# Kernel tuning notes

Measured on AMD Instinct MI355X. Metric: run time of the kernel, lower is better.

Reference implementation:

```python
import jax, jax.numpy as jnp
import numpy as np

E, H2, V = 128, 512, 50000  # embedding_size, hidden_size*2, output_size
H4 = 2 * H2


def _gru_cell(x, h, W_ih, W_hh, b_ih, b_hh):
    # PyTorch GRU cell: gates ordered (r, z, n)
    gi = x @ W_ih.T + b_ih
    gh = h @ W_hh.T + b_hh
    i_r, i_z, i_n = jnp.split(gi, 3, axis=-1)
    h_r, h_z, h_n = jnp.split(gh, 3, axis=-1)
    r = jax.nn.sigmoid(i_r + h_r)
    z = jax.nn.sigmoid(i_z + h_z)
    n = jnp.tanh(i_n + r * h_n)
    return (1.0 - z) * n + z * h


def setup_inputs() -> dict:
    key = jax.random.key(0)
    ks = jax.random.split(key, 24)
    B, T = 64, 400
    s = 0.02
    inp = {
        "input_ids": jax.random.randint(ks[0], (B, 1), 0, V),
        "pre_hidden": jax.random.normal(ks[1], (2, B, H2), jnp.float32),
        "encoder_outputs": jax.random.normal(ks[2], (B, T, H2), jnp.float32),
        "source_input": jax.random.randint(ks[3], (B, T), 0, V),
        "coverage_vector": jax.random.uniform(ks[4], (B, 1, T), jnp.float32),
        "emb_table": jax.random.normal(ks[5], (V, E), jnp.float32) * s,
        "W_ih0": jax.random.normal(ks[6], (3 * H2, E), jnp.float32) * s,
        "W_hh0": jax.random.normal(ks[7], (3 * H2, H2), jnp.float32) * s,
        "b_ih0": jnp.zeros((3 * H2,), jnp.float32),
        "b_hh0": jnp.zeros((3 * H2,), jnp.float32),
        "W_ih1": jax.random.normal(ks[8], (3 * H2, H2), jnp.float32) * s,
        "W_hh1": jax.random.normal(ks[9], (3 * H2, H2), jnp.float32) * s,
        "b_ih1": jnp.zeros((3 * H2,), jnp.float32),
        "b_hh1": jnp.zeros((3 * H2,), jnp.float32),
        "align_W": jax.random.normal(ks[10], (1, 3 * H2), jnp.float32) * s,
        "align_b": jnp.zeros((1,), jnp.float32),
        "cov_W": jax.random.normal(ks[11], (H2, 1), jnp.float32) * s,
        "cov_b": jnp.zeros((H2,), jnp.float32),
        "fc1_W": jax.random.normal(ks[12], (H4, H4), jnp.float32) * s,
        "fc1_b": jnp.zeros((H4,), jnp.float32),
        "fc2_W": jax.random.normal(ks[13], (V, H4), jnp.float32) * s,
        "fc2_b": jnp.zeros((V,), jnp.float32),
        "gen_W": jax.random.normal(ks[14], (1, H4 + E), jnp.float32) * s,
        "gen_b": jnp.zeros((1,), jnp.float32),
    }
    return inp


def reference(input_ids, pre_hidden, encoder_outputs, source_input, coverage_vector,
              emb_table, W_ih0, W_hh0, b_ih0, b_hh0, W_ih1, W_hh1, b_ih1, b_hh1,
              align_W, align_b, cov_W, cov_b, fc1_W, fc1_b, fc2_W, fc2_b, gen_W, gen_b):
    B, T = source_input.shape
    # embedding lookup (dropout omitted / eval mode)
    emb = emb_table[input_ids[:, 0]]                          # [B,E]
    # 2-layer GRU, single decode step
    h0 = _gru_cell(emb, pre_hidden[0], W_ih0, W_hh0, b_ih0, b_hh0)
    h1 = _gru_cell(h0, pre_hidden[1], W_ih1, W_hh1, b_ih1, b_hh1)
    current_hidden = jnp.stack([h0, h1], axis=0)              # [2,B,H2]
    s = h1                                                    # [B,H2]
    cov = coverage_vector[:, 0, :]                            # [B,T]
    # coverage projection: Linear(1 -> H2)
    cov_feat = cov[:, :, None] * cov_W[:, 0][None, None, :] + cov_b  # [B,T,H2]
    s_rep = jnp.broadcast_to(s[:, None, :], (B, T, s.shape[-1]))
    combine = jnp.concatenate([encoder_outputs, s_rep, cov_feat], axis=-1)  # [B,T,3*H2]
    scores = jnp.einsum('bti,i->bt', combine, align_W[0]) + align_b[0]
    attn = jax.nn.softmax(jnp.tanh(scores), axis=1)           # [B,T]
    # coverage loss: sum of elementwise min(attn, coverage)
    coverage_loss = jnp.sum(jnp.minimum(attn, cov))
    new_coverage = coverage_vector + attn[:, None, :]         # [B,1,T]
    context = jnp.einsum('bt,bth->bh', attn, encoder_outputs) # [B,H2]
    ni = jnp.tanh(jnp.concatenate([s, context], axis=-1) @ fc1_W.T + fc1_b)
    logits = ni @ fc2_W.T + fc2_b                             # [B,V]
    Pvocab = jax.nn.softmax(logits, axis=1)
    # vectorized copy distribution: scatter-add attention mass onto source token ids
    batch_idx = jnp.arange(B)[:, None]
    copy_prob = jnp.zeros((B, logits.shape[1]), logits.dtype).at[batch_idx, source_input].add(attn)
    gen_in = jnp.concatenate([context, s, emb], axis=-1)      # [B,H4+E]
    p_gen = jax.nn.sigmoid(gen_in @ gen_W.T + gen_b)          # [B,1]
    out = Pvocab * p_gen + copy_prob * (1.0 - p_gen)
    return (out, current_hidden, attn[:, None, :], copy_prob, new_coverage, coverage_loss)
```

## Files before the change

### kernel.cpp

```cpp
#include <hip/hip_runtime.h>
#include <hip/hip_bf16.h>
#include <cstddef>

#define BB 64
#define TT 400
#define EE 128
#define HH 512
#define H4 1024
#define VV 50000
#define NCH 8
#define LSTR 136

#define OFF_OUT     0
#define OFF_CURHID  (BB*VV)
#define OFF_ATTN    (OFF_CURHID + 2*BB*HH)
#define OFF_COPY    (OFF_ATTN + BB*TT)
#define OFF_NEWCOV  (OFF_COPY + BB*VV)
#define OFF_LOSS    (OFF_NEWCOV + BB*TT)

#define WS_S      0
#define WS_TS     (WS_S + BB*HH)
#define WS_ATTN   (WS_TS + BB*TT)
#define WS_NIB    (WS_ATTN + BB*TT)
#define WS_A1     (WS_NIB + BB*H4/2)
#define WS_AX0    (WS_A1 + BB*H4/2)
#define WS_AH0    (WS_AX0 + BB*EE/2)
#define WS_AH1    (WS_AH0 + BB*HH/2)
#define WS_AX1    (WS_AH1 + BB*HH/2)
#define WS_PGEN   (WS_AX1 + BB*HH/2)
#define WS_RM     (WS_PGEN + 64)
#define WS_RS     (WS_RM + 64)
#define WS_CTXP   (WS_RS + 64)
#define WS_LOGITS (WS_CTXP + BB*NCH*HH)

typedef __attribute__((ext_vector_type(8))) short short8v;
typedef __attribute__((ext_vector_type(4))) short short4v;
typedef __attribute__((ext_vector_type(4))) float f32x4;

__device__ __forceinline__ float wredsum(float v) {
#pragma unroll
  for (int o = 32; o > 0; o >>= 1) v += __shfl_down(v, o, 64);
  return v;
}
__device__ __forceinline__ float wredmax(float v) {
#pragma unroll
  for (int o = 32; o > 0; o >>= 1) v = fmaxf(v, __shfl_down(v, o, 64));
  return v;
}
__device__ __forceinline__ float dot4(float4 a, float4 b) {
  return a.x*b.x + a.y*b.y + a.z*b.z + a.w*b.w;
}
__device__ __forceinline__ float sigmoidf(float x) { return 1.f / (1.f + expf(-x)); }
__device__ __forceinline__ short bfh(float f) {
  union { __hip_bfloat16 h; short s; } u; u.h = __float2bfloat16(f); return u.s;
}
__device__ __forceinline__ float bf2f(short s) {
  union { unsigned int u; float f; } v; v.u = ((unsigned int)(unsigned short)s) << 16; return v.f;
}

__global__ void zero_prep_kernel(float* __restrict__ p, float* __restrict__ loss,
                                 float* __restrict__ rs,
                                 const float* __restrict__ embt, const int* __restrict__ ids,
                                 const float* __restrict__ preh,
                                 short* __restrict__ ax0, short* __restrict__ ah0,
                                 short* __restrict__ ah1) {
  int i = blockIdx.x * 256 + threadIdx.x;
  ((float4*)p)[i] = make_float4(0.f, 0.f, 0.f, 0.f);
  if (i == 0) loss[0] = 0.f;
  if (i < 64) rs[i] = 0.f;
  if (i < BB * EE) {
    int b = i >> 7, k = i & 127;
    ax0[i] = bfh(embt[(size_t)ids[b] * EE + k]);
  } else if (i < BB * EE + 2 * BB * HH) {
    int j = i - BB * EE;
    if (j < BB * HH) ah0[j] = bfh(preh[j]);
    else ah1[j - BB * HH] = bfh(preh[j]);
  }
}

template<int KX>
__global__ __launch_bounds__(768) void gru_mfma_kernel(
    const short* __restrict__ Ax, const short* __restrict__ Ah,
    const float* __restrict__ W_ih, const float* __restrict__ W_hh,
    const float* __restrict__ b_ih, const float* __restrict__ b_hh,
    const float* __restrict__ hprev,
    float* __restrict__ hout_f, float* __restrict__ hout_o,
    short* __restrict__ hout_b, int bstride) {
  __shared__ float Pf[12 * 256];
  const int w = threadIdx.x >> 6;
  const int lane = threadIdx.x & 63;
  const int r16 = lane & 15, kg = lane >> 4;
  const int j0 = (blockIdx.x & 31) * 16;
  const int bg = blockIdx.x >> 5;
  const int half = (w >= 6) ? 1 : 0;
  const int wv = w - half * 6;
  const int part = (wv >= 3) ? 1 : 0;
  const int g = wv - part * 3;
  const int K = part ? HH : KX;
  const int Kh = K >> 1;
  const float* Wm = part ? W_hh : W_ih;
  const short* Am = part ? Ah : Ax;

  f32x4 acc = {0.f, 0.f, 0.f, 0.f};
  const float* wp = Wm + (size_t)(g * HH + j0 + r16) * K + half * Kh + kg * 8;
  const short* ap = Am + (size_t)(bg * 16 + r16) * K + half * Kh + kg * 8;
#pragma unroll 4
  for (int k0 = 0; k0 < Kh; k0 += 32) {
    float4 w0 = *(const float4*)(wp + k0);
    float4 w1 = *(const float4*)(wp + k0 + 4);
    short8v a = *(const short8v*)(ap + k0);
    short8v bf;
    bf[0] = bfh(w0.x); bf[1] = bfh(w0.y); bf[2] = bfh(w0.z); bf[3] = bfh(w0.w);
    bf[4] = bfh(w1.x); bf[5] = bfh(w1.y); bf[6] = bfh(w1.z); bf[7] = bfh(w1.w);
    acc = __builtin_amdgcn_mfma_f32_16x16x32_bf16(a, bf, acc, 0, 0, 0);
  }
  float* pw = Pf + (half * 6 + part * 3 + g) * 256;
#pragma unroll
  for (int r = 0; r < 4; r++) pw[(kg * 4 + r) * 16 + r16] = acc[r];
  __syncthreads();
  if (w == 0) {
    int col = j0 + r16;
    float bir = b_ih[col] + b_hh[col];
    float biz = b_ih[HH + col] + b_hh[HH + col];
    float bin = b_ih[2 * HH + col], bhn = b_hh[2 * HH + col];
#pragma unroll
    for (int r = 0; r < 4; r++) {
      int m = kg * 4 + r;
      int row = bg * 16 + m;
      int o = m * 16 + r16;
      float ih_r = Pf[0 * 256 + o] + Pf[6 * 256 + o];
      float ih_z = Pf[1 * 256 + o] + Pf[7 * 256 + o];
      float ih_n = Pf[2 * 256 + o] + Pf[8 * 256 + o];
      float hh_r = Pf[3 * 256 + o] + Pf[9 * 256 + o];
      float hh_z = Pf[4 * 256 + o] + Pf[10 * 256 + o];
      float hh_n = Pf[5 * 256 + o] + Pf[11 * 256 + o];
      float rv = sigmoidf(ih_r + hh_r + bir);
      float zv = sigmoidf(ih_z + hh_z + biz);
      float nv = tanhf(ih_n + bin + rv * (hh_n + bhn));
      float h = (1.f - zv) * nv + zv * hprev[(size_t)row * HH + col];
      hout_f[(size_t)row * HH + col] = h;
      hout_o[(size_t)row * HH + col] = h;
      hout_b[(size_t)row * bstride + col] = bfh(h);
    }
  }
}

__global__ void scores_kernel(const float* __restrict__ enc, const float* __restrict__ cov,
                              const float* __restrict__ aW, const float* __restrict__ ab,
                              const float* __restrict__ covW, const float* __restrict__ covb,
                              const float* __restrict__ s, float* __restrict__ ts) {
  int b = blockIdx.y;
  int wid = threadIdx.x >> 6, lane = threadIdx.x & 63;
  int t = blockIdx.x * 4 + wid;
  int i8 = lane * 8;
  const float* e = enc + ((size_t)b * TT + t) * HH + i8;
  float4 a0 = *(const float4*)&aW[i8],        a1 = *(const float4*)&aW[i8 + 4];
  float4 b0 = *(const float4*)&aW[HH + i8],   b1 = *(const float4*)&aW[HH + i8 + 4];
  float4 c0 = *(const float4*)&aW[2*HH + i8], c1 = *(const float4*)&aW[2*HH + i8 + 4];
  float4 s0 = *(const float4*)&s[(size_t)b * HH + i8], s1 = *(const float4*)&s[(size_t)b * HH + i8 + 4];
  float4 w0 = *(const float4*)&covW[i8],      w1 = *(const float4*)&covW[i8 + 4];
  float4 v0 = *(const float4*)&covb[i8],      v1 = *(const float4*)&covb[i8 + 4];
  float covbt = cov[b * TT + t];
  float p1 = dot4(*(const float4*)&e[0], a0) + dot4(*(const float4*)&e[4], a1)
           + dot4(s0, b0) + dot4(s1, b1)
           + dot4(v0, c0) + dot4(v1, c1);
  float p2 = dot4(w0, c0) + dot4(w1, c1);
  float d = wredsum(p1 + covbt * p2);
  if (lane == 0) ts[b * TT + t] = tanhf(d + ab[0]);
}

__global__ void attn_kernel(const float* __restrict__ ts, const float* __restrict__ cov,
                            const int* __restrict__ src,
                            float* __restrict__ wattn, float* __restrict__ dout,
                            float* __restrict__ outc) {
  int b = blockIdx.x, tid = threadIdx.x;
  int lane = tid & 63, wid = tid >> 6;
  __shared__ float sred[8];
  __shared__ float bval[2];
  float v = (tid < TT) ? ts[b * TT + tid] : -1e30f;
  float wm = wredmax(v);
  if (lane == 0) sred[wid] = wm;
  __syncthreads();
  if (wid == 0) {
    float r = (lane < 8) ? sred[lane] : -1e30f;
    r = wredmax(r);
    if (lane == 0) bval[0] = r;
  }
  __syncthreads();
  float m = bval[0];
  float e = (tid < TT) ? expf(v - m) : 0.f;
  float wsm = wredsum(e);
  __syncthreads();
  if (lane == 0) sred[wid] = wsm;
  __syncthreads();
  if (wid == 0) {
    float r = (lane < 8) ? sred[lane] : 0.f;
    r = wredsum(r);
    if (lane == 0) bval[1] = r;
  }
  __syncthreads();
  float denom = bval[1];
  float a = e / denom;
  float lp = 0.f;
  if (tid < TT) {
    wattn[b * TT + tid] = a;
    dout[OFF_ATTN + b * TT + tid] = a;
    float c = cov[b * TT + tid];
    dout[OFF_NEWCOV + b * TT + tid] = c + a;
    lp = fminf(a, c);
    atomicAdd(&outc[(size_t)b * VV + src[b * TT + tid]], a);
  }
  float wl = wredsum(lp);
  __syncthreads();
  if (lane == 0) sred[wid] = wl;
  __syncthreads();
  if (wid == 0) {
    float r = (lane < 8) ? sred[lane] : 0.f;
    r = wredsum(r);
    if (lane == 0) atomicAdd(&dout[OFF_LOSS], r);
  }
}

__global__ void ctx_part_kernel(const float* __restrict__ enc, const float* __restrict__ attn,
                                float* __restrict__ ctxp) {
  int b = blockIdx.x, c = blockIdx.y;
  int h = threadIdx.x;
  __shared__ float as[TT / NCH];
  if (h < TT / NCH) as[h] = attn[b * TT + c * (TT / NCH) + h];
  __syncthreads();
  const float* e = enc + ((size_t)b * TT + c * (TT / NCH)) * HH + h;
  float acc = 0.f;
#pragma unroll 10
  for (int t = 0; t < TT / NCH; t++) acc += as[t] * e[(size_t)t * HH];
  ctxp[((size_t)b * NCH + c) * HH + h] = acc;
}

__global__ void ctxred_pgen_kernel(const float* __restrict__ ctxp, const float* __restrict__ s,
                                   const float* __restrict__ embt, const int* __restrict__ ids,
                                   const float* __restrict__ gW, const float* __restrict__ gb,
                                   short* __restrict__ a1, float* __restrict__ pgen) {
  int b = blockIdx.x, tid = threadIdx.x;
  int lane = tid & 63, wid = tid >> 6;
  __shared__ float sred[8];
  float acc = 0.f;
#pragma unroll
  for (int c = 0; c < NCH; c++) acc += ctxp[((size_t)b * NCH + c) * HH + tid];
  a1[(size_t)b * H4 + HH + tid] = bfh(acc);
  float part = acc * gW[tid] + s[b * HH + tid] * gW[HH + tid];
  if (tid < EE) part += embt[(size_t)ids[b] * EE + tid] * gW[2 * HH + tid];
  float w = wredsum(part);
  if (lane == 0) sred[wid] = w;
  __syncthreads();
  if (wid == 0) {
    float r = (lane < 8) ? sred[lane] : 0.f;
    r = wredsum(r);
    if (lane == 0) pgen[b] = sigmoidf(r + gb[0]);
  }
}

__global__ __launch_bounds__(256) void fc1_kernel(const short* __restrict__ a1,
                                                  const float* __restrict__ W,
                                                  const float* __restrict__ bias,
                                                  short* __restrict__ nib) {
  __shared__ float part[4096];
  const int w = threadIdx.x >> 6;
  const int lane = threadIdx.x & 63;
  const int r16 = lane & 15, kg = lane >> 4;
  const int v0 = blockIdx.x * 16;
  const int kb = w * 256;

  f32x4 acc0 = {0.f,0.f,0.f,0.f}, acc1 = {0.f,0.f,0.f,0.f};
  f32x4 acc2 = {0.f,0.f,0.f,0.f}, acc3 = {0.f,0.f,0.f,0.f};
  const float* wp = W + (size_t)(v0 + r16) * H4 + kb + kg * 8;
  const short* ap = a1 + (size_t)r16 * H4 + kb + kg * 8;
#pragma unroll 4
  for (int k0 = 0; k0 < 256; k0 += 32) {
    float4 w0 = *(const float4*)(wp + k0);
    float4 w1 = *(const float4*)(wp + k0 + 4);
    short8v a0 = *(const short8v*)(ap + k0);
    short8v a1v = *(const short8v*)(ap + 16 * H4 + k0);
    short8v a2 = *(const short8v*)(ap + 32 * H4 + k0);
    short8v a3 = *(const short8v*)(ap + 48 * H4 + k0);
    short8v bf;
    bf[0] = bfh(w0.x); bf[1] = bfh(w0.y); bf[2] = bfh(w0.z); bf[3] = bfh(w0.w);
    bf[4] = bfh(w1.x); bf[5] = bfh(w1.y); bf[6] = bfh(w1.z); bf[7] = bfh(w1.w);
    acc0 = __builtin_amdgcn_mfma_f32_16x16x32_bf16(a0, bf, acc0, 0, 0, 0);
    acc1 = __builtin_amdgcn_mfma_f32_16x16x32_bf16(a1v, bf, acc1, 0, 0, 0);
    acc2 = __builtin_amdgcn_mfma_f32_16x16x32_bf16(a2, bf, acc2, 0, 0, 0);
    acc3 = __builtin_amdgcn_mfma_f32_16x16x32_bf16(a3, bf, acc3, 0, 0, 0);
  }
  float* pb = part + w * 1024;
#pragma unroll
  for (int r = 0; r < 4; r++) {
    pb[(kg * 4 + r) * 16 + r16]      = acc0[r];
    pb[(16 + kg * 4 + r) * 16 + r16] = acc1[r];
    pb[(32 + kg * 4 + r) * 16 + r16] = acc2[r];
    pb[(48 + kg * 4 + r) * 16 + r16] = acc3[r];
  }
  __syncthreads();
  int idx = threadIdx.x * 4;
  int m = idx >> 4, c0 = idx & 15;
  f32x4 s0 = *(const f32x4*)(part + idx);
  f32x4 s1 = *(const f32x4*)(part + 1024 + idx);
  f32x4 s2 = *(const f32x4*)(part + 2048 + idx);
  f32x4 s3 = *(const f32x4*)(part + 3072 + idx);
  f32x4 bv = *(const f32x4*)(bias + v0 + c0);
  f32x4 o = s0 + s1 + s2 + s3 + bv;
#pragma unroll
  for (int j = 0; j < 4; j++)
    nib[(size_t)m * H4 + v0 + c0 + j] = bfh(tanhf(o[j]));
}

__global__ __launch_bounds__(256) void fc2_kernel(const short* __restrict__ nib,
                                                  const float* __restrict__ W,
                                                  const float* __restrict__ bias,
                                                  short* __restrict__ logits_bf,
                                                  float* __restrict__ rs) {
  __shared__ short Wl[64 * LSTR];
  __shared__ short Al[64 * LSTR];
  const int tid = threadIdx.x;
  const int w = tid >> 6, lane = tid & 63;
  const int r16 = lane & 15, kg = lane >> 4;
  const int v0 = blockIdx.x * 64;
  const int srow = tid >> 2, quad = tid & 3;
  const int vr = min(v0 + srow, VV - 1);

  f32x4 acc[4];
#pragma unroll
  for (int i = 0; i < 4; i++) acc[i] = (f32x4){0.f, 0.f, 0.f, 0.f};

  const float* wsrc = W + (size_t)vr * H4 + quad * 4;
  const short* asrc = nib + (size_t)srow * H4 + quad * 8;

  float4 wreg[8];
  short8v areg[4];
#pragma unroll
  for (int j = 0; j < 8; j++) wreg[j] = *(const float4*)(wsrc + j * 16);
#pragma unroll
  for (int j = 0; j < 4; j++) areg[j] = *(const short8v*)(asrc + j * 32);

  for (int ks = 0; ks < 8; ks++) {
    {
      char* dst = (char*)Wl + srow * (LSTR * 2) + quad * 8;
#pragma unroll
      for (int j = 0; j < 8; j++) {
        float4 f = wreg[j];
        short4v h; h[0] = bfh(f.x); h[1] = bfh(f.y); h[2] = bfh(f.z); h[3] = bfh(f.w);
        *(short4v*)(dst + j * 32) = h;
      }
      char* adst = (char*)Al + srow * (LSTR * 2) + quad * 16;
#pragma unroll
      for (int j = 0; j < 4; j++)
        *(short8v*)(adst + j * 64) = areg[j];
    }
    __syncthreads();
    if (ks < 7) {
      const float* ws2 = wsrc + (ks + 1) * 128;
      const short* as2 = asrc + (ks + 1) * 128;
#pragma unroll
      for (int j = 0; j < 8; j++) wreg[j] = *(const float4*)(ws2 + j * 16);
#pragma unroll
      for (int j = 0; j < 4; j++) areg[j] = *(const short8v*)(as2 + j * 32);
    }
#pragma unroll
    for (int s = 0; s < 4; s++) {
      short8v wf = *(const short8v*)((char*)Wl + (w * 16 + r16) * (LSTR * 2) + s * 64 + kg * 16);
#pragma unroll
      for (int i = 0; i < 4; i++) {
        short8v af = *(const short8v*)((char*)Al + (i * 16 + r16) * (LSTR * 2) + s * 64 + kg * 16);
        acc[i] = __builtin_amdgcn_mfma_f32_16x16x32_bf16(af, wf, acc[i], 0, 0, 0);
      }
    }
    __syncthreads();
  }

  float* sc = (float*)Wl;
#pragma unroll
  for (int i = 0; i < 4; i++)
#pragma unroll
    for (int r = 0; r < 4; r++)
      sc[(i * 16 + kg * 4 + r) * 64 + w * 16 + r16] = acc[i][r];
  __syncthreads();
  int m = tid >> 2, q = tid & 3;
  int colbase = v0 + q * 16;
  float esum = 0.f;
  if (colbase < VV) {
    const float* scp = sc + m * 64 + q * 16;
    short8v lo, hi;
#pragma unroll
    for (int j = 0; j < 8; j++) {
      short lb = bfh(scp[j] + bias[colbase + j]);
      lo[j] = lb;
      esum += expf(bf2f(lb));
    }
#pragma unroll
    for (int j = 0; j < 8; j++) {
      short lb = bfh(scp[8 + j] + bias[colbase + 8 + j]);
      hi[j] = lb;
      esum += expf(bf2f(lb));
    }
    *(short8v*)(logits_bf + (size_t)m * VV + colbase)     = lo;
    *(short8v*)(logits_bf + (size_t)m * VV + colbase + 8) = hi;
  }
  esum += __shfl_down(esum, 2, 4);
  esum += __shfl_down(esum, 1, 4);
  if (q == 0) atomicAdd(&rs[m], esum);
}

__global__ void final_kernel(const short* __restrict__ logits_bf, const float* __restrict__ rs,
                             const float* __restrict__ pgen,
                             const float* __restrict__ copy, float* __restrict__ out) {
  int i = blockIdx.x * 256 + threadIdx.x;
  int b = (i * 4) / VV;
  float p = pgen[b], s = rs[b];
  short4v l = ((const short4v*)logits_bf)[i];
  float4 c = ((const float4*)copy)[i];
  float q = 1.f - p;
  float ps = p / s;
  float4 o;
  o.x = expf(bf2f(l[0])) * ps + c.x * q;
  o.y = expf(bf2f(l[1])) * ps + c.y * q;
  o.z = expf(bf2f(l[2])) * ps + c.z * q;
  o.w = expf(bf2f(l[3])) * ps + c.w * q;
  ((float4*)out)[i] = o;
}

extern "C" void kernel_launch(void* const* d_in, const int* in_sizes, int n_in,
                              void* d_out, int out_size, void* d_ws, size_t ws_size,
                              hipStream_t stream) {
  const int*   ids  = (const int*)d_in[0];
  const float* preh = (const float*)d_in[1];
  const float* enc  = (const float*)d_in[2];
  const int*   src  = (const int*)d_in[3];
  const float* cov  = (const float*)d_in[4];
  const float* embt = (const float*)d_in[5];
  const float* Wih0 = (const float*)d_in[6];
  const float* Whh0 = (const float*)d_in[7];
  const float* bih0 = (const float*)d_in[8];
  const float* bhh0 = (const float*)d_in[9];
  const float* Wih1 = (const float*)d_in[10];
  const float* Whh1 = (const float*)d_in[11];
  const float* bih1 = (const float*)d_in[12];
  const float* bhh1 = (const float*)d_in[13];
  const float* aW   = (const float*)d_in[14];
  const float* ab   = (const float*)d_in[15];
  const float* covW = (const float*)d_in[16];
  const float* covb = (const float*)d_in[17];
  const float* f1W  = (const float*)d_in[18];
  const float* f1b  = (const float*)d_in[19];
  const float* f2W  = (const float*)d_in[20];
  const float* f2b  = (const float*)d_in[21];
  const float* gW   = (const float*)d_in[22];
  const float* gb   = (const float*)d_in[23];
  float* out = (float*)d_out;
  float* ws  = (float*)d_ws;

  zero_prep_kernel<<<3125, 256, 0, stream>>>(out + OFF_COPY, out + OFF_LOSS, ws + WS_RS,
                                             embt, ids, preh,
                                             (short*)(ws + WS_AX0), (short*)(ws + WS_AH0),
                                             (short*)(ws + WS_AH1));
  gru_mfma_kernel<EE><<<128, 768, 0, stream>>>(
      (const short*)(ws + WS_AX0), (const short*)(ws + WS_AH0),
      Wih0, Whh0, bih0, bhh0, preh,
      out + OFF_CURHID, out + OFF_CURHID, (short*)(ws + WS_AX1), HH);
  gru_mfma_kernel<HH><<<128, 768, 0, stream>>>(
      (const short*)(ws + WS_AX1), (const short*)(ws + WS_AH1),
      Wih1, Whh1, bih1, bhh1, preh + BB * HH,
      ws + WS_S, out + OFF_CURHID + BB * HH, (short*)(ws + WS_A1), H4);
  scores_kernel<<<dim3(100, 64), 256, 0, stream>>>(enc, cov, aW, ab, covW, covb,
                                                   ws + WS_S, ws + WS_TS);
  attn_kernel<<<64, 512, 0, stream>>>(ws + WS_TS, cov, src, ws + WS_ATTN, out,
                                      out + OFF_COPY);
  ctx_part_kernel<<<dim3(64, NCH), 512, 0, stream>>>(enc, ws + WS_ATTN, ws + WS_CTXP);
  ctxred_pgen_kernel<<<64, 512, 0, stream>>>(ws + WS_CTXP, ws + WS_S, embt, ids, gW, gb,
                                             (short*)(ws + WS_A1), ws + WS_PGEN);
  fc1_kernel<<<64, 256, 0, stream>>>((const short*)(ws + WS_A1), f1W, f1b,
                                     (short*)(ws + WS_NIB));
  fc2_kernel<<<782, 256, 0, stream>>>((const short*)(ws + WS_NIB), f2W, f2b,
                                      (short*)(ws + WS_LOGITS), ws + WS_RS);
  final_kernel<<<3125, 256, 0, stream>>>((const short*)(ws + WS_LOGITS), ws + WS_RS,
                                         ws + WS_PGEN, out + OFF_COPY, out);
}
```

Before: 127.8 us.

## Split attention score, hoist encoder dot into prep kernel, double-buffer fc2 weights

The attention score is split algebraically: the encoder·align_W part only depends on inputs, so it is computed early in the zero/prep kernel. The hidden-state and coverage terms reduce to per-batch scalars computed inside attn_kernel, which removes the separate scores_kernel launch and takes it off the GRU-dependent critical path. Separately, fc2 now keeps two register buffers of weights so global loads run two k-steps ahead. The cost is more register pressure in fc2 and a heavier prep kernel that now reads all of encoder_outputs.

```diff
diff --git a/kernel.cpp b/kernel.cpp
--- a/kernel.cpp
+++ b/kernel.cpp
@@ -19,8 +19,8 @@
 #define OFF_LOSS    (OFF_NEWCOV + BB*TT)
 
 #define WS_S      0
-#define WS_TS     (WS_S + BB*HH)
-#define WS_ATTN   (WS_TS + BB*TT)
+#define WS_ESC    (WS_S + BB*HH)
+#define WS_ATTN   (WS_ESC + BB*TT)
 #define WS_NIB    (WS_ATTN + BB*TT)
 #define WS_A1     (WS_NIB + BB*H4/2)
 #define WS_AX0    (WS_A1 + BB*H4/2)
@@ -62,8 +62,9 @@
                                  float* __restrict__ rs,
                                  const float* __restrict__ embt, const int* __restrict__ ids,
                                  const float* __restrict__ preh,
+                                 const float* __restrict__ enc, const float* __restrict__ aW,
                                  short* __restrict__ ax0, short* __restrict__ ah0,
-                                 short* __restrict__ ah1) {
+                                 short* __restrict__ ah1, float* __restrict__ esc) {
   int i = blockIdx.x * 256 + threadIdx.x;
   ((float4*)p)[i] = make_float4(0.f, 0.f, 0.f, 0.f);
   if (i == 0) loss[0] = 0.f;
@@ -75,6 +76,17 @@
     int j = i - BB * EE;
     if (j < BB * HH) ah0[j] = bfh(preh[j]);
     else ah1[j - BB * HH] = bfh(preh[j]);
+  }
+  int wgid = blockIdx.x * 4 + (threadIdx.x >> 6);
+  int lane = threadIdx.x & 63;
+  int i8 = lane * 8;
+  float4 a0 = *(const float4*)&aW[i8];
+  float4 a1 = *(const float4*)&aW[i8 + 4];
+  for (int idx = wgid; idx < BB * TT; idx += 12500) {
+    const float* e = enc + (size_t)idx * HH + i8;
+    float d = dot4(*(const float4*)&e[0], a0) + dot4(*(const float4*)&e[4], a1);
+    d = wredsum(d);
+    if (lane == 0) esc[idx] = d;
   }
 }
 
@@ -145,39 +157,35 @@
   }
 }
 
-__global__ void scores_kernel(const float* __restrict__ enc, const float* __restrict__ cov,
-                              const float* __restrict__ aW, const float* __restrict__ ab,
-                              const float* __restrict__ covW, const float* __restrict__ covb,
-                              const float* __restrict__ s, float* __restrict__ ts) {
-  int b = blockIdx.y;
-  int wid = threadIdx.x >> 6, lane = threadIdx.x & 63;
-  int t = blockIdx.x * 4 + wid;
-  int i8 = lane * 8;
-  const float* e = enc + ((size_t)b * TT + t) * HH + i8;
-  float4 a0 = *(const float4*)&aW[i8],        a1 = *(const float4*)&aW[i8 + 4];
-  float4 b0 = *(const float4*)&aW[HH + i8],   b1 = *(const float4*)&aW[HH + i8 + 4];
-  float4 c0 = *(const float4*)&aW[2*HH + i8], c1 = *(const float4*)&aW[2*HH + i8 + 4];
-  float4 s0 = *(const float4*)&s[(size_t)b * HH + i8], s1 = *(const float4*)&s[(size_t)b * HH + i8 + 4];
-  float4 w0 = *(const float4*)&covW[i8],      w1 = *(const float4*)&covW[i8 + 4];
-  float4 v0 = *(const float4*)&covb[i8],      v1 = *(const float4*)&covb[i8 + 4];
-  float covbt = cov[b * TT + t];
-  float p1 = dot4(*(const float4*)&e[0], a0) + dot4(*(const float4*)&e[4], a1)
-           + dot4(s0, b0) + dot4(s1, b1)
-           + dot4(v0, c0) + dot4(v1, c1);
-  float p2 = dot4(w0, c0) + dot4(w1, c1);
-  float d = wredsum(p1 + covbt * p2);
-  if (lane == 0) ts[b * TT + t] = tanhf(d + ab[0]);
-}
-
-__global__ void attn_kernel(const float* __restrict__ ts, const float* __restrict__ cov,
-                            const int* __restrict__ src,
+__global__ void attn_kernel(const float* __restrict__ esc, const float* __restrict__ cov,
+                            const int* __restrict__ src, const float* __restrict__ s,
+                            const float* __restrict__ aW, const float* __restrict__ ab,
+                            const float* __restrict__ covW, const float* __restrict__ covb,
                             float* __restrict__ wattn, float* __restrict__ dout,
                             float* __restrict__ outc) {
   int b = blockIdx.x, tid = threadIdx.x;
   int lane = tid & 63, wid = tid >> 6;
-  __shared__ float sred[8];
-  __shared__ float bval[2];
-  float v = (tid < TT) ? ts[b * TT + tid] : -1e30f;
+  __shared__ float sred[24];
+  __shared__ float bval[8];
+  {
+    float a2 = aW[2 * HH + tid];
+    float p1 = s[(size_t)b * HH + tid] * aW[HH + tid];
+    float p2 = covW[tid] * a2;
+    float p3 = covb[tid] * a2;
+    float r1 = wredsum(p1), r2 = wredsum(p2), r3 = wredsum(p3);
+    if (lane == 0) { sred[wid] = r1; sred[8 + wid] = r2; sred[16 + wid] = r3; }
+    __syncthreads();
+    if (wid == 0) {
+      float q1 = (lane < 8) ? sred[lane] : 0.f;      q1 = wredsum(q1);
+      float q2 = (lane < 8) ? sred[8 + lane] : 0.f;  q2 = wredsum(q2);
+      float q3 = (lane < 8) ? sred[16 + lane] : 0.f; q3 = wredsum(q3);
+      if (lane == 0) { bval[2] = q1; bval[3] = q2; bval[4] = q3 + ab[0]; }
+    }
+    __syncthreads();
+  }
+  float sdot = bval[2], c1 = bval[3], c0 = bval[4];
+  float cvt = (tid < TT) ? cov[b * TT + tid] : 0.f;
+  float v = (tid < TT) ? tanhf(esc[b * TT + tid] + sdot + cvt * c1 + c0) : -1e30f;
   float wm = wredmax(v);
   if (lane == 0) sred[wid] = wm;
   __syncthreads();
@@ -205,9 +213,8 @@
   if (tid < TT) {
     wattn[b * TT + tid] = a;
     dout[OFF_ATTN + b * TT + tid] = a;
-    float c = cov[b * TT + tid];
-    dout[OFF_NEWCOV + b * TT + tid] = c + a;
-    lp = fminf(a, c);
+    dout[OFF_NEWCOV + b * TT + tid] = cvt + a;
+    lp = fminf(a, cvt);
     atomicAdd(&outc[(size_t)b * VV + src[b * TT + tid]], a);
   }
   float wl = wredsum(lp);
@@ -332,35 +339,35 @@
   const float* wsrc = W + (size_t)vr * H4 + quad * 4;
   const short* asrc = nib + (size_t)srow * H4 + quad * 8;
 
-  float4 wreg[8];
+  float4 wregA[8], wregB[8];
   short8v areg[4];
 #pragma unroll
-  for (int j = 0; j < 8; j++) wreg[j] = *(const float4*)(wsrc + j * 16);
+  for (int j = 0; j < 8; j++) wregA[j] = *(const float4*)(wsrc + j * 16);
+#pragma unroll
+  for (int j = 0; j < 8; j++) wregB[j] = *(const float4*)(wsrc + 128 + j * 16);
 #pragma unroll
   for (int j = 0; j < 4; j++) areg[j] = *(const short8v*)(asrc + j * 32);
 
-  for (int ks = 0; ks < 8; ks++) {
-    {
-      char* dst = (char*)Wl + srow * (LSTR * 2) + quad * 8;
-#pragma unroll
-      for (int j = 0; j < 8; j++) {
-        float4 f = wreg[j];
-        short4v h; h[0] = bfh(f.x); h[1] = bfh(f.y); h[2] = bfh(f.z); h[3] = bfh(f.w);
-        *(short4v*)(dst + j * 32) = h;
-      }
-      char* adst = (char*)Al + srow * (LSTR * 2) + quad * 16;
-#pragma unroll
-      for (int j = 0; j < 4; j++)
-        *(short8v*)(adst + j * 64) = areg[j];
-    }
+  auto step = [&](float4 (&wcur)[8], int ks) {
+    char* dst = (char*)Wl + srow * (LSTR * 2) + quad * 8;
+#pragma unroll
+    for (int j = 0; j < 8; j++) {
+      float4 f = wcur[j];
+      short4v h; h[0] = bfh(f.x); h[1] = bfh(f.y); h[2] = bfh(f.z); h[3] = bfh(f.w);
+      *(short4v*)(dst + j * 32) = h;
+    }
+    char* adst = (char*)Al + srow * (LSTR * 2) + quad * 16;
+#pragma unroll
+    for (int j = 0; j < 4; j++)
+      *(short8v*)(adst + j * 64) = areg[j];
     __syncthreads();
+    if (ks < 6) {
+#pragma unroll
+      for (int j = 0; j < 8; j++) wcur[j] = *(const float4*)(wsrc + (ks + 2) * 128 + j * 16);
+    }
     if (ks < 7) {
-      const float* ws2 = wsrc + (ks + 1) * 128;
-      const short* as2 = asrc + (ks + 1) * 128;
-#pragma unroll
-      for (int j = 0; j < 8; j++) wreg[j] = *(const float4*)(ws2 + j * 16);
-#pragma unroll
-      for (int j = 0; j < 4; j++) areg[j] = *(const short8v*)(as2 + j * 32);
+#pragma unroll
+      for (int j = 0; j < 4; j++) areg[j] = *(const short8v*)(asrc + (ks + 1) * 128 + j * 32);
     }
 #pragma unroll
     for (int s = 0; s < 4; s++) {
@@ -372,6 +379,11 @@
       }
     }
     __syncthreads();
+  };
+#pragma unroll
+  for (int it = 0; it < 4; it++) {
+    step(wregA, 2 * it);
+    step(wregB, 2 * it + 1);
   }
 
   float* sc = (float*)Wl;
@@ -456,9 +468,9 @@
   float* ws  = (float*)d_ws;
 
   zero_prep_kernel<<<3125, 256, 0, stream>>>(out + OFF_COPY, out + OFF_LOSS, ws + WS_RS,
-                                             embt, ids, preh,
+                                             embt, ids, preh, enc, aW,
                                              (short*)(ws + WS_AX0), (short*)(ws + WS_AH0),
-                                             (short*)(ws + WS_AH1));
+                                             (short*)(ws + WS_AH1), ws + WS_ESC);
   gru_mfma_kernel<EE><<<128, 768, 0, stream>>>(
       (const short*)(ws + WS_AX0), (const short*)(ws + WS_AH0),
       Wih0, Whh0, bih0, bhh0, preh,
@@ -467,10 +479,9 @@
       (const short*)(ws + WS_AX1), (const short*)(ws + WS_AH1),
       Wih1, Whh1, bih1, bhh1, preh + BB * HH,
       ws + WS_S, out + OFF_CURHID + BB * HH, (short*)(ws + WS_A1), H4);
-  scores_kernel<<<dim3(100, 64), 256, 0, stream>>>(enc, cov, aW, ab, covW, covb,
-                                                   ws + WS_S, ws + WS_TS);
-  attn_kernel<<<64, 512, 0, stream>>>(ws + WS_TS, cov, src, ws + WS_ATTN, out,
-                                      out + OFF_COPY);
+  attn_kernel<<<64, 512, 0, stream>>>(ws + WS_ESC, cov, src, ws + WS_S,
+                                      aW, ab, covW, covb,
+                                      ws + WS_ATTN, out, out + OFF_COPY);
   ctx_part_kernel<<<dim3(64, NCH), 512, 0, stream>>>(enc, ws + WS_ATTN, ws + WS_CTXP);
   ctxred_pgen_kernel<<<64, 512, 0, stream>>>(ws + WS_CTXP, ws + WS_S, embt, ids, gW, gb,
                                              (short*)(ws + WS_A1), ws + WS_PGEN);
```

Result: faster. 122.4 us (-4.2%).
